# Kernel tuning notes

Hardware: AMD Instinct MI355X
Metric: run time of the kernel (lower is better)

Reference implementation:

```python
import jax, jax.numpy as jnp
import numpy as np

B, D, N, M = 64, 128, 400, 50
H, KD = 8, 16
NCONV, K, PAD = 4, 7, 3
MAXTS = 10000.0


def _pe(l):
    # PositionEncoding: freqs/phases interleave sin/cos as sin(pos*f + phase)
    i = np.arange(D)
    freqs = MAXTS ** np.where(i % 2 == 0, -i / D, -(i - 1) / D)
    phases = np.where(i % 2 == 0, 0.0, np.pi / 2)
    pos = np.arange(l)
    return jnp.asarray(np.sin(pos[None, :] * freqs[:, None] + phases[:, None]).astype(np.float32))  # [D, l]


def _ln(x, g, b, eps=1e-6):
    # LayerNorm1d over channel dim of [B, D, L]; torch .std() is unbiased (ddof=1), divides by (std+eps)
    mu = x.mean(axis=1, keepdims=True)
    sd = x.std(axis=1, keepdims=True, ddof=1)
    return g[None, :, None] * (x - mu) / (sd + eps) + b[None, :, None]


def _attn(xT, mask, Wq, bq, Wk, bk, Wv, bv, Wo, bo):
    # xT: [B, L, D]; per-head linears vectorized over the head axis
    q = jnp.einsum('bld,hdk->bhlk', xT, Wq) + bq[None, :, None, :]
    k = jnp.einsum('bld,hdk->bhlk', xT, Wk) + bk[None, :, None, :]
    v = jnp.einsum('bld,hdk->bhlk', xT, Wv) + bv[None, :, None, :]
    sc = jnp.einsum('bhik,bhjk->bhij', q, k) / np.sqrt(KD)
    sc = sc - 1e30 * (1.0 - mask[:, None, None, :])  # mask over key positions
    a = jax.nn.softmax(sc, axis=-1)
    o = jnp.einsum('bhij,bhjk->bhik', a, v)
    o = o.transpose(0, 2, 1, 3).reshape(xT.shape[0], xT.shape[1], H * KD)
    return o @ Wo + bo


def _fwd(context_emb, question_emb, c_mask, q_mask, ln_g, ln_b, dw_w, dw_b, pw_w, pw_b,
         Wq, bq, Wk, bk, Wv, bv, Wo, bo, Wfc, bfc, cq_wc, cq_wq, cq_wm, cq_b):
    def block(x, mask):
        out = x + _pe(x.shape[2])[None]
        for i in range(NCONV):  # fixed small layer loop
            res = out
            h = _ln(out, ln_g, ln_b)
            h = jax.lax.conv_general_dilated(h, dw_w[i], (1,), [(PAD, PAD)],
                                             feature_group_count=D,
                                             dimension_numbers=('NCH', 'OIH', 'NCH')) + dw_b[i][None, :, None]
            h = jnp.einsum('bdl,ed->bel', h, pw_w[i]) + pw_b[i][None, :, None]
            out = jax.nn.relu(h) + res  # eval-mode layer_dropout = inputs + residual
        res = out
        h = _ln(out, ln_g, ln_b)
        h = _attn(h.transpose(0, 2, 1), mask, Wq, bq, Wk, bk, Wv, bv, Wo, bo)
        out = h.transpose(0, 2, 1) + res
        res = out
        h = _ln(out, ln_g, ln_b)
        h = jnp.einsum('bdl,ed->bel', h, Wfc) + bfc[None, :, None]
        return h + res

    C = block(context_emb, c_mask)
    Q = block(question_emb, q_mask)
    C2 = C.transpose(0, 2, 1)  # [B, N, D]
    Q2 = Q.transpose(0, 2, 1)  # [B, M, D]
    # Biaffine similarity W0([Q; C; Q*C]) decomposed (same math, no [B,N*M,3D] materialization)
    S = (C2 @ cq_wc)[:, :, None] + (Q2 @ cq_wq)[:, None, :] \
        + jnp.einsum('bnd,bmd->bnm', C2 * cq_wm, Q2) + cq_b[0]
    S_r = jax.nn.softmax(S - 1e30 * (1.0 - q_mask[:, None, :]), axis=2)
    S_c = jax.nn.softmax(S - 1e30 * (1.0 - c_mask[:, :, None]), axis=1)
    A = S_r @ Q2                                    # context-to-query [B, N, D]
    Bt = jnp.einsum('bnm,bkm->bnk', S_r, S_c) @ C2  # query-to-context (DCN style) [B, N, D]
    return jnp.concatenate([C2, A, C2 * A, C2 * Bt], axis=-1)  # [B, N, 4D]


def setup_inputs() -> dict:
    key = jax.random.key(0)
    ks = jax.random.split(key, 16)
    s = 1.0 / np.sqrt(D)
    return dict(
        context_emb=jax.random.normal(ks[0], (B, D, N), jnp.float32),
        question_emb=jax.random.normal(ks[1], (B, D, M), jnp.float32),
        c_mask=jnp.ones((B, N), jnp.float32),
        q_mask=jnp.ones((B, M), jnp.float32),
        ln_g=jnp.ones((D,), jnp.float32),
        ln_b=jnp.zeros((D,), jnp.float32),
        dw_w=jax.random.normal(ks[2], (NCONV, D, 1, K), jnp.float32) / np.sqrt(K),
        dw_b=jnp.zeros((NCONV, D), jnp.float32),
        pw_w=jax.random.normal(ks[3], (NCONV, D, D), jnp.float32) * s,
        pw_b=jnp.zeros((NCONV, D), jnp.float32),
        Wq=jax.random.normal(ks[4], (H, D, KD), jnp.float32) * s,
        bq=jnp.zeros((H, KD), jnp.float32),
        Wk=jax.random.normal(ks[5], (H, D, KD), jnp.float32) * s,
        bk=jnp.zeros((H, KD), jnp.float32),
        Wv=jax.random.normal(ks[6], (H, D, KD), jnp.float32) * s,
        bv=jnp.zeros((H, KD), jnp.float32),
        Wo=jax.random.normal(ks[7], (H * KD, D), jnp.float32) * s,
        bo=jnp.zeros((D,), jnp.float32),
        Wfc=jax.random.normal(ks[8], (D, D), jnp.float32) * s,
        bfc=jnp.zeros((D,), jnp.float32),
        cq_wc=jax.random.normal(ks[9], (D,), jnp.float32) * s,
        cq_wq=jax.random.normal(ks[10], (D,), jnp.float32) * s,
        cq_wm=jax.random.normal(ks[11], (D,), jnp.float32) * s,
        cq_b=jnp.zeros((1,), jnp.float32),
    )


def reference(context_emb, question_emb, c_mask, q_mask, ln_g, ln_b, dw_w, dw_b, pw_w, pw_b,
              Wq, bq, Wk, bk, Wv, bv, Wo, bo, Wfc, bfc, cq_wc, cq_wq, cq_wm, cq_b):
    return _fwd(context_emb, question_emb, c_mask, q_mask, ln_g, ln_b, dw_w, dw_b, pw_w, pw_b,
                Wq, bq, Wk, bk, Wv, bv, Wo, bo, Wfc, bfc, cq_wc, cq_wq, cq_wm, cq_b)
```

## Files before the change

### kernel.cpp

```cpp
#include <hip/hip_runtime.h>
#include <math.h>

#define BB 64
#define DD 128
#define NN 400
#define MM 50
#define HH 8
#define KDIM 16
#define NC 4
#define KW 7
#define CH 200

#define SZ_C (BB * DD * NN)
#define SZ_Q (BB * DD * MM)
#define SSTAT (BB * NN + BB * MM)

__global__ void k_transposeW(const float* __restrict__ pw_w, const float* __restrict__ Wo,
                             const float* __restrict__ Wfc, const float* __restrict__ Wq,
                             const float* __restrict__ Wk, const float* __restrict__ Wv,
                             float* __restrict__ Wcan) {
  int idx = blockIdx.x * 256 + threadIdx.x;
  if (idx >= 9 * 16384) return;
  int m = idx >> 14;
  int r = idx & 16383;
  int d = r >> 7, e = r & 127;
  float v;
  if (m < 4) v = pw_w[m * 16384 + e * 128 + d];
  else if (m == 4) v = Wo[d * 128 + e];
  else if (m == 5) v = Wfc[e * 128 + d];
  else {
    const float* W = (m == 6) ? Wq : (m == 7) ? Wk : Wv;
    v = W[((e >> 4) * 128 + d) * 16 + (e & 15)];
  }
  Wcan[idx] = v;
}

__global__ void k_pestats(const float* __restrict__ xC, const float* __restrict__ xQ,
                          float* __restrict__ yC, float* __restrict__ yQ,
                          float* __restrict__ mu, float* __restrict__ inv) {
  int blk = blockIdx.x;
  const float* x; float* y; int L, l0, b, soff;
  if (blk < 448) { b = blk / 7; l0 = (blk % 7) * 64; x = xC; y = yC; L = NN; soff = 0; }
  else { b = blk - 448; l0 = 0; x = xQ; y = yQ; L = MM; soff = BB * NN; }
  int tid = threadIdx.x;
  int ll = tid & 63;
  int dq = tid >> 6;
  int l = l0 + ll;
  __shared__ float s_sum[4][64], s_sq[4][64];
  float sum = 0.f, sq = 0.f;
  if (l < L) {
    const float* px = x + (size_t)b * DD * L + l;
    float* py = y + (size_t)b * DD * L + l;
    for (int d = dq * 32; d < dq * 32 + 32; ++d) {
      int de = d & ~1;
      float freq = __expf((float)de * (-9.210340371976184f / 128.0f));
      float ph = (d & 1) ? 1.5707963267948966f : 0.0f;
      float v = px[(size_t)d * L] + sinf((float)l * freq + ph);
      py[(size_t)d * L] = v;
      sum += v; sq += v * v;
    }
  }
  s_sum[dq][ll] = sum; s_sq[dq][ll] = sq;
  __syncthreads();
  if (dq == 0 && l < L) {
    float ts = s_sum[0][ll] + s_sum[1][ll] + s_sum[2][ll] + s_sum[3][ll];
    float tq = s_sq[0][ll] + s_sq[1][ll] + s_sq[2][ll] + s_sq[3][ll];
    float m = ts * (1.0f / 128.0f);
    float var = (tq - 128.0f * m * m) * (1.0f / 127.0f);
    float sd = sqrtf(fmaxf(var, 0.f));
    mu[soff + b * L + l] = m;
    inv[soff + b * L + l] = 1.0f / (sd + 1e-6f);
  }
}

__global__ __launch_bounds__(256, 2) void k_convgemm(
    const float* __restrict__ xC, const float* __restrict__ xQ,
    float* __restrict__ outC, float* __restrict__ outQ,
    const float* __restrict__ Wc, const float* __restrict__ pwb,
    const float* __restrict__ dww, const float* __restrict__ dwb,
    const float* __restrict__ muI, const float* __restrict__ invI,
    float* __restrict__ muO, float* __restrict__ invO,
    const float* __restrict__ g, const float* __restrict__ beta) {
  int blk = blockIdx.x;
  int b = blk >> 3, tile = blk & 7;
  const float* x; float* out; int L, l0, soff;
  if (tile < 7) { x = xC; out = outC; L = NN; l0 = tile * 64; soff = 0; }
  else { x = xQ; out = outQ; L = MM; l0 = 0; soff = BB * NN; }
  __shared__ float Wl[32 * 128];
  __shared__ float Xl[32 * 64];
  __shared__ float Sm[70], Si[70];
  int tid = threadIdx.x;
  const float* xb = x + (size_t)b * DD * L;
  for (int t = tid; t < 70; t += 256) {
    int gl = l0 + t - 3;
    bool ok = (gl >= 0 && gl < L);
    Sm[t] = ok ? muI[soff + b * L + gl] : 0.f;
    Si[t] = ok ? invI[soff + b * L + gl] : 0.f;
  }
  float acc[8][4];
  #pragma unroll
  for (int i = 0; i < 8; ++i)
    #pragma unroll
    for (int j = 0; j < 4; ++j) acc[i][j] = 0.f;
  __syncthreads();
  for (int kc = 0; kc < 4; ++kc) {
    int d0 = kc * 32;
    #pragma unroll
    for (int i = 0; i < 4; ++i) {
      int idx = i * 256 + tid;
      ((float4*)Wl)[idx] = ((const float4*)Wc)[(size_t)d0 * 32 + idx];
    }
    #pragma unroll
    for (int r = 0; r < 2; ++r) {
      int k = r * 16 + (tid >> 4);
      int d = d0 + k;
      int c0 = (tid & 15) * 4;
      const float* xrow = xb + (size_t)d * L;
      float gd = g[d], bd = beta[d];
      float wv[7];
      #pragma unroll
      for (int u = 0; u < 7; ++u) wv[u] = dww[d * 7 + u];
      float dbv = dwb[d];
      float xw[10];
      int gbase = l0 + c0 - 3;
      if (gbase >= 1 && gbase + 11 <= L && (((unsigned)(d * L + gbase - 1)) & 3u) == 0u) {
        const float4* p = (const float4*)&xrow[gbase - 1];
        float4 A = p[0], Bv = p[1], Cv = p[2];
        float xr[12] = {A.x, A.y, A.z, A.w, Bv.x, Bv.y, Bv.z, Bv.w, Cv.x, Cv.y, Cv.z, Cv.w};
        #pragma unroll
        for (int s = 0; s < 10; ++s)
          xw[s] = gd * (xr[s + 1] - Sm[c0 + s]) * Si[c0 + s] + bd;
      } else {
        #pragma unroll
        for (int s = 0; s < 10; ++s) {
          int gl = gbase + s;
          float v = 0.f;
          if (gl >= 0 && gl < L)
            v = gd * (xrow[gl] - Sm[c0 + s]) * Si[c0 + s] + bd;
          xw[s] = v;
        }
      }
      float4 o;
      o.x = dbv; o.y = dbv; o.z = dbv; o.w = dbv;
      #pragma unroll
      for (int u = 0; u < 7; ++u) {
        o.x += wv[u] * xw[u];
        o.y += wv[u] * xw[u + 1];
        o.z += wv[u] * xw[u + 2];
        o.w += wv[u] * xw[u + 3];
      }
      *(float4*)&Xl[k * 64 + c0] = o;
    }
    __syncthreads();
    int e0 = (tid >> 4) * 8, cq = (tid & 15) * 4;
    for (int k = 0; k < 32; ++k) {
      const float4* wp = (const float4*)&Wl[k * 128 + e0];
      float4 w0 = wp[0], w1 = wp[1];
      float4 xv = *(const float4*)&Xl[k * 64 + cq];
      float we[8] = {w0.x, w0.y, w0.z, w0.w, w1.x, w1.y, w1.z, w1.w};
      float xe[4] = {xv.x, xv.y, xv.z, xv.w};
      #pragma unroll
      for (int i = 0; i < 8; ++i)
        #pragma unroll
        for (int j = 0; j < 4; ++j) acc[i][j] += we[i] * xe[j];
    }
    __syncthreads();
  }
  int e0 = (tid >> 4) * 8, cq = (tid & 15) * 4;
  float ssum[4], ssq[4];
  #pragma unroll
  for (int j = 0; j < 4; ++j) { ssum[j] = 0.f; ssq[j] = 0.f; }
  #pragma unroll
  for (int i = 0; i < 8; ++i) {
    float bi = pwb[e0 + i];
    float* po = out + ((size_t)b * DD + e0 + i) * L;
    const float* pr = xb + (size_t)(e0 + i) * L;
    #pragma unroll
    for (int j = 0; j < 4; ++j) {
      int l = l0 + cq + j;
      if (l < L) {
        float v = fmaxf(acc[i][j] + bi, 0.f) + pr[l];
        po[l] = v;
        ssum[j] += v; ssq[j] += v * v;
      }
    }
  }
  int grp = tid >> 4;
  #pragma unroll
  for (int j = 0; j < 4; ++j) {
    Xl[grp * 64 + cq + j] = ssum[j];
    Wl[grp * 64 + cq + j] = ssq[j];
  }
  __syncthreads();
  if (tid < 64) {
    int l = l0 + tid;
    if (l < L) {
      float ts = 0.f, tq = 0.f;
      #pragma unroll
      for (int gg = 0; gg < 16; ++gg) { ts += Xl[gg * 64 + tid]; tq += Wl[gg * 64 + tid]; }
      float m = ts * (1.0f / 128.0f);
      float var = (tq - 128.0f * m * m) * (1.0f / 127.0f);
      float sd = sqrtf(fmaxf(var, 0.f));
      muO[soff + b * L + l] = m;
      invO[soff + b * L + l] = 1.0f / (sd + 1e-6f);
    }
  }
}

template <int LNF, int ACT, int STATS>
__global__ __launch_bounds__(256) void k_gemm64(
    const float* __restrict__ xC, const float* __restrict__ xQ,
    float* __restrict__ outC, float* __restrict__ outQ,
    const float* __restrict__ Wc, const float* __restrict__ bias,
    const float* __restrict__ mu, const float* __restrict__ inv,
    float* __restrict__ muO, float* __restrict__ invO,
    const float* __restrict__ g, const float* __restrict__ beta) {
  int blk = blockIdx.x;
  int b = blk >> 3, tile = blk & 7;
  const float* x; float* out; int L, l0, soff;
  if (tile < 7) { x = xC; out = outC; L = NN; l0 = tile * 64; soff = 0; }
  else { x = xQ; out = outQ; L = MM; l0 = 0; soff = BB * NN; }
  __shared__ float Wl[32 * 128];
  __shared__ float Xl[32 * 64];
  int tid = threadIdx.x;
  float acc[8][4];
  #pragma unroll
  for (int i = 0; i < 8; ++i)
    #pragma unroll
    for (int j = 0; j < 4; ++j) acc[i][j] = 0.f;
  const float* xb = x + (size_t)b * DD * L;
  const float* pmu = mu + soff + b * L;
  const float* pin = inv + soff + b * L;
  for (int kc = 0; kc < 4; ++kc) {
    int d0 = kc * 32;
    #pragma unroll
    for (int i = 0; i < 4; ++i) {
      int idx = i * 256 + tid;
      ((float4*)Wl)[idx] = ((const float4*)Wc)[(size_t)d0 * 32 + idx];
    }
    #pragma unroll
    for (int t = 0; t < 8; ++t) {
      int idx = t * 256 + tid;
      int k = idx >> 6, l = idx & 63;
      float v = 0.f;
      int gl = l0 + l;
      if (gl < L) {
        v = xb[(size_t)(d0 + k) * L + gl];
        if (LNF) v = g[d0 + k] * (v - pmu[gl]) * pin[gl] + beta[d0 + k];
      }
      Xl[idx] = v;
    }
    __syncthreads();
    int e0 = (tid >> 4) * 8, cq = (tid & 15) * 4;
    for (int k = 0; k < 32; ++k) {
      const float4* wp = (const float4*)&Wl[k * 128 + e0];
      float4 w0 = wp[0], w1 = wp[1];
      float4 xv = *(const float4*)&Xl[k * 64 + cq];
      float we[8] = {w0.x, w0.y, w0.z, w0.w, w1.x, w1.y, w1.z, w1.w};
      float xe[4] = {xv.x, xv.y, xv.z, xv.w};
      #pragma unroll
      for (int i = 0; i < 8; ++i)
        #pragma unroll
        for (int j = 0; j < 4; ++j) acc[i][j] += we[i] * xe[j];
    }
    __syncthreads();
  }
  int e0 = (tid >> 4) * 8, cq = (tid & 15) * 4;
  float ssum[4], ssq[4];
  #pragma unroll
  for (int j = 0; j < 4; ++j) { ssum[j] = 0.f; ssq[j] = 0.f; }
  #pragma unroll
  for (int i = 0; i < 8; ++i) {
    float bi = bias[e0 + i];
    float* po = out + ((size_t)b * DD + e0 + i) * L;
    #pragma unroll
    for (int j = 0; j < 4; ++j) {
      int l = l0 + cq + j;
      if (l < L) {
        float v = acc[i][j] + bi;
        if (ACT != 0) v += po[l];
        po[l] = v;
        if (STATS) { ssum[j] += v; ssq[j] += v * v; }
      }
    }
  }
  if (STATS) {
    int grp = tid >> 4;
    #pragma unroll
    for (int j = 0; j < 4; ++j) {
      Xl[grp * 64 + cq + j] = ssum[j];
      Wl[grp * 64 + cq + j] = ssq[j];
    }
    __syncthreads();
    if (tid < 64) {
      int l = l0 + tid;
      if (l < L) {
        float ts = 0.f, tq = 0.f;
        #pragma unroll
        for (int gg = 0; gg < 16; ++gg) { ts += Xl[gg * 64 + tid]; tq += Wl[gg * 64 + tid]; }
        float m = ts * (1.0f / 128.0f);
        float var = (tq - 128.0f * m * m) * (1.0f / 127.0f);
        float sd = sqrtf(fmaxf(var, 0.f));
        muO[soff + b * L + l] = m;
        invO[soff + b * L + l] = 1.0f / (sd + 1e-6f);
      }
    }
  }
}

__global__ __launch_bounds__(256) void k_gemm_qkv(
    const float* __restrict__ xC, const float* __restrict__ xQ,
    float* __restrict__ o1C, float* __restrict__ o1Q,
    float* __restrict__ o2C, float* __restrict__ o2Q,
    float* __restrict__ o3C, float* __restrict__ o3Q,
    const float* __restrict__ Wcan,
    const float* __restrict__ bq, const float* __restrict__ bk, const float* __restrict__ bv,
    const float* __restrict__ mu, const float* __restrict__ inv,
    const float* __restrict__ g, const float* __restrict__ beta) {
  int blk0 = blockIdx.x;
  int grp = blk0 >> 9;
  int blk = blk0 & 511;
  const float* Wc = Wcan + (size_t)(6 + grp) * 16384;
  const float* bias = (grp == 0) ? bq : (grp == 1) ? bk : bv;
  float* oC = (grp == 0) ? o1C : (grp == 1) ? o2C : o3C;
  float* oQ = (grp == 0) ? o1Q : (grp == 1) ? o2Q : o3Q;
  int b = blk >> 3, tile = blk & 7;
  const float* x; float* out; int L, l0, soff;
  if (tile < 7) { x = xC; out = oC; L = NN; l0 = tile * 64; soff = 0; }
  else { x = xQ; out = oQ; L = MM; l0 = 0; soff = BB * NN; }
  __shared__ float Wl[32 * 128];
  __shared__ float Xl[32 * 64];
  int tid = threadIdx.x;
  float acc[8][4];
  #pragma unroll
  for (int i = 0; i < 8; ++i)
    #pragma unroll
    for (int j = 0; j < 4; ++j) acc[i][j] = 0.f;
  const float* xb = x + (size_t)b * DD * L;
  const float* pmu = mu + soff + b * L;
  const float* pin = inv + soff + b * L;
  for (int kc = 0; kc < 4; ++kc) {
    int d0 = kc * 32;
    #pragma unroll
    for (int i = 0; i < 4; ++i) {
      int idx = i * 256 + tid;
      ((float4*)Wl)[idx] = ((const float4*)Wc)[(size_t)d0 * 32 + idx];
    }
    #pragma unroll
    for (int t = 0; t < 8; ++t) {
      int idx = t * 256 + tid;
      int k = idx >> 6, l = idx & 63;
      float v = 0.f;
      int gl = l0 + l;
      if (gl < L) {
        v = xb[(size_t)(d0 + k) * L + gl];
        v = g[d0 + k] * (v - pmu[gl]) * pin[gl] + beta[d0 + k];
      }
      Xl[idx] = v;
    }
    __syncthreads();
    int e0 = (tid >> 4) * 8, cq = (tid & 15) * 4;
    for (int k = 0; k < 32; ++k) {
      const float4* wp = (const float4*)&Wl[k * 128 + e0];
      float4 w0 = wp[0], w1 = wp[1];
      float4 xv = *(const float4*)&Xl[k * 64 + cq];
      float we[8] = {w0.x, w0.y, w0.z, w0.w, w1.x, w1.y, w1.z, w1.w};
      float xe[4] = {xv.x, xv.y, xv.z, xv.w};
      #pragma unroll
      for (int i = 0; i < 8; ++i)
        #pragma unroll
        for (int j = 0; j < 4; ++j) acc[i][j] += we[i] * xe[j];
    }
    __syncthreads();
  }
  int e0 = (tid >> 4) * 8, cq = (tid & 15) * 4;
  #pragma unroll
  for (int i = 0; i < 8; ++i) {
    float bi = bias[e0 + i];
    float* po = out + ((size_t)b * DD + e0 + i) * L;
    #pragma unroll
    for (int j = 0; j < 4; ++j) {
      int l = l0 + cq + j;
      if (l < L) po[l] = acc[i][j] + bi;
    }
  }
}

__global__ __launch_bounds__(256) void k_attn2(
    const float* __restrict__ qC, const float* __restrict__ kC, const float* __restrict__ vC,
    const float* __restrict__ qQ, const float* __restrict__ kQ, const float* __restrict__ vQ,
    const float* __restrict__ cmask, const float* __restrict__ qmask,
    float* __restrict__ oC, float* __restrict__ oQ) {
  int blk = blockIdx.x;
  const float *qp, *kp, *vp, *mk; float* op; int L, b, h, q0, qcnt;
  if (blk < 1024) {
    b = blk >> 4; h = (blk >> 1) & 7; int half = blk & 1;
    qp = qC; kp = kC; vp = vC; mk = cmask; op = oC; L = NN;
    q0 = half * 256; qcnt = half ? (NN - 256) : 256;
  } else {
    int bb = blk - 1024; b = bb >> 3; h = bb & 7;
    qp = qQ; kp = kQ; vp = vQ; mk = qmask; op = oQ; L = MM;
    q0 = 0; qcnt = MM;
  }
  __shared__ float Kl[CH * KDIM];
  __shared__ float Vl[CH * KDIM];
  __shared__ float Ml[CH + 8];
  int tid = threadIdx.x;
  size_t base = ((size_t)b * DD + h * KDIM) * L;
  bool act = tid < qcnt;
  int i = q0 + tid;
  float q[KDIM];
  #pragma unroll
  for (int t = 0; t < KDIM; ++t)
    q[t] = act ? qp[base + (size_t)t * L + i] * 0.25f : 0.f;
  float m = -1e30f, ls = 0.f;
  float acc[KDIM];
  #pragma unroll
  for (int t = 0; t < KDIM; ++t) acc[t] = 0.f;

  for (int c0 = 0; c0 < L; c0 += CH) {
    int ch = L - c0; if (ch > CH) ch = CH;
    int chp = (ch + 7) & ~7;
    const float* kpc = kp + base + c0;
    const float* vpc = vp + base + c0;
    for (int idx = tid; idx < KDIM * ch; idx += 256) {
      int t = idx / ch, j = idx - t * ch;
      Kl[j * KDIM + t] = kpc[(size_t)t * L + j];
      Vl[j * KDIM + t] = vpc[(size_t)t * L + j];
    }
    for (int idx = tid; idx < (chp - ch) * KDIM; idx += 256) {
      int j = ch + (idx >> 4), t = idx & 15;
      Kl[j * KDIM + t] = 0.f; Vl[j * KDIM + t] = 0.f;
    }
    for (int j = tid; j < chp; j += 256)
      Ml[j] = (j < ch) ? -1e30f * (1.0f - mk[b * L + c0 + j]) : -1e30f;
    __syncthreads();
    if (act) {
      for (int j0 = 0; j0 < chp; j0 += 8) {
        const float4* mp = (const float4*)&Ml[j0];
        float4 ma0 = mp[0], ma1 = mp[1];
        float mav[8] = {ma0.x, ma0.y, ma0.z, ma0.w, ma1.x, ma1.y, ma1.z, ma1.w};
        float s[8];
        #pragma unroll
        for (int jj = 0; jj < 8; ++jj) {
          const float4* kf = (const float4*)&Kl[(j0 + jj) * KDIM];
          float4 k0 = kf[0], k1 = kf[1], k2 = kf[2], k3 = kf[3];
          float da = q[0] * k0.x + q[1] * k0.y + q[2] * k0.z + q[3] * k0.w
                   + q[4] * k1.x + q[5] * k1.y + q[6] * k1.z + q[7] * k1.w;
          float db = q[8] * k2.x + q[9] * k2.y + q[10] * k2.z + q[11] * k2.w
                   + q[12] * k3.x + q[13] * k3.y + q[14] * k3.z + q[15] * k3.w;
          s[jj] = da + db + mav[jj];
        }
        float cm = s[0];
        #pragma unroll
        for (int jj = 1; jj < 8; ++jj) cm = fmaxf(cm, s[jj]);
        if (cm > m) {
          float sc = __expf(m - cm);
          ls *= sc;
          #pragma unroll
          for (int t = 0; t < KDIM; ++t) acc[t] *= sc;
          m = cm;
        }
        #pragma unroll
        for (int jj = 0; jj < 8; ++jj) {
          float p = __expf(s[jj] - m);
          ls += p;
          const float4* vf = (const float4*)&Vl[(j0 + jj) * KDIM];
          float4 v0 = vf[0], v1 = vf[1], v2 = vf[2], v3 = vf[3];
          acc[0] += p * v0.x;  acc[1] += p * v0.y;  acc[2] += p * v0.z;  acc[3] += p * v0.w;
          acc[4] += p * v1.x;  acc[5] += p * v1.y;  acc[6] += p * v1.z;  acc[7] += p * v1.w;
          acc[8] += p * v2.x;  acc[9] += p * v2.y;  acc[10] += p * v2.z; acc[11] += p * v2.w;
          acc[12] += p * v3.x; acc[13] += p * v3.y; acc[14] += p * v3.z; acc[15] += p * v3.w;
        }
      }
    }
    __syncthreads();
  }
  if (act) {
    float invl = 1.0f / ls;
    #pragma unroll
    for (int t = 0; t < KDIM; ++t)
      op[base + (size_t)t * L + i] = acc[t] * invl;
  }
}

__global__ void k_prep(const float* __restrict__ Cb, const float* __restrict__ Qb,
                       float* __restrict__ C2, float* __restrict__ Q2,
                       const float* __restrict__ wc, const float* __restrict__ wq,
                       float* __restrict__ cd, float* __restrict__ qd) {
  int blk = blockIdx.x, tid = threadIdx.x;
  if (blk < 3840) {
    const float* X; float* Y; int L, rem;
    if (blk < 3328) { X = Cb; Y = C2; L = NN; rem = blk; }
    else { X = Qb; Y = Q2; L = MM; rem = blk - 3328; }
    int ntl = (L + 31) / 32;
    int b = rem / (4 * ntl);
    int r2 = rem % (4 * ntl);
    int d0 = (r2 / ntl) * 32;
    int l0 = (r2 % ntl) * 32;
    __shared__ float T[32][33];
    int c = tid & 31, r8 = tid >> 5;
    const float* xb = X + (size_t)b * DD * L;
    #pragma unroll
    for (int k = 0; k < 4; ++k) {
      int r = r8 + k * 8;
      int l = l0 + c;
      T[r][c] = (l < L) ? xb[(size_t)(d0 + r) * L + l] : 0.f;
    }
    __syncthreads();
    float* yb = Y + (size_t)b * L * DD;
    #pragma unroll
    for (int k = 0; k < 4; ++k) {
      int rr = r8 + k * 8;
      int l = l0 + rr;
      if (l < L) yb[(size_t)l * DD + d0 + c] = T[c][rr];
    }
  } else if (blk < 3940) {
    int idx = (blk - 3840) * 256 + tid;
    if (idx < BB * NN) {
      int l = idx % NN, b = idx / NN;
      const float* px = Cb + (size_t)b * DD * NN + l;
      float acc = 0.f;
      for (int d = 0; d < DD; ++d) acc += px[(size_t)d * NN] * wc[d];
      cd[idx] = acc;
    }
  } else {
    int idx = (blk - 3940) * 256 + tid;
    if (idx < BB * MM) {
      int l = idx % MM, b = idx / MM;
      const float* px = Qb + (size_t)b * DD * MM + l;
      float acc = 0.f;
      for (int d = 0; d < DD; ++d) acc += px[(size_t)d * MM] * wq[d];
      qd[idx] = acc;
    }
  }
}

__global__ void k_S(const float* __restrict__ C2, const float* __restrict__ Q2,
                    const float* __restrict__ cd, const float* __restrict__ qd,
                    const float* __restrict__ wm, const float* __restrict__ bias,
                    float* __restrict__ S) {
  int idx = blockIdx.x * 256 + threadIdx.x;
  if (idx >= BB * NN * MM) return;
  int mcol = idx % MM;
  int n = (idx / MM) % NN;
  int b = idx / (MM * NN);
  const float4* pc = (const float4*)(C2 + ((size_t)b * NN + n) * DD);
  const float4* pq = (const float4*)(Q2 + ((size_t)b * MM + mcol) * DD);
  const float4* pw = (const float4*)wm;
  float a0 = 0.f, a1 = 0.f;
  #pragma unroll 4
  for (int d4 = 0; d4 < 32; d4 += 2) {
    float4 c0 = pc[d4], w0 = pw[d4], q0 = pq[d4];
    float4 c1 = pc[d4 + 1], w1 = pw[d4 + 1], q1 = pq[d4 + 1];
    a0 += (c0.x * w0.x) * q0.x + (c0.y * w0.y) * q0.y + (c0.z * w0.z) * q0.z + (c0.w * w0.w) * q0.w;
    a1 += (c1.x * w1.x) * q1.x + (c1.y * w1.y) * q1.y + (c1.z * w1.z) * q1.z + (c1.w * w1.w) * q1.w;
  }
  S[idx] = a0 + a1 + cd[b * NN + n] + qd[b * MM + mcol] + bias[0];
}

__global__ void k_smax(const float* __restrict__ S, float* __restrict__ Sr,
                       float* __restrict__ Sc, const float* __restrict__ cmask,
                       const float* __restrict__ qmask) {
  int blk = blockIdx.x;
  int tid = threadIdx.x;
  if (blk < BB * MM) {
    int b = blk / MM;
    int mcol = blk % MM;
    float vals[7];
    float mx = -1e30f;
    #pragma unroll
    for (int c = 0; c < 7; ++c) {
      int n = tid + c * 64;
      float s = -1e30f;
      if (n < NN)
        s = S[((size_t)b * NN + n) * MM + mcol] - 1e30f * (1.0f - cmask[b * NN + n]);
      vals[c] = s;
      mx = fmaxf(mx, s);
    }
    #pragma unroll
    for (int off = 1; off < 64; off <<= 1) mx = fmaxf(mx, __shfl_xor(mx, off));
    float sum = 0.f;
    #pragma unroll
    for (int c = 0; c < 7; ++c) { vals[c] = __expf(vals[c] - mx); sum += vals[c]; }
    #pragma unroll
    for (int off = 1; off < 64; off <<= 1) sum += __shfl_xor(sum, off);
    float inv = 1.0f / sum;
    #pragma unroll
    for (int c = 0; c < 7; ++c) {
      int n = tid + c * 64;
      if (n < NN) Sc[((size_t)b * NN + n) * MM + mcol] = vals[c] * inv;
    }
  } else {
    int bn = blk - BB * MM;
    int b = bn / NN;
    float s = -1e30f;
    if (tid < MM)
      s = S[(size_t)bn * MM + tid] - 1e30f * (1.0f - qmask[b * MM + tid]);
    float mx = s;
    #pragma unroll
    for (int off = 1; off < 64; off <<= 1) mx = fmaxf(mx, __shfl_xor(mx, off));
    float e = (tid < MM) ? __expf(s - mx) : 0.f;
    float sum = e;
    #pragma unroll
    for (int off = 1; off < 64; off <<= 1) sum += __shfl_xor(sum, off);
    if (tid < MM) Sr[(size_t)bn * MM + tid] = e / sum;
  }
}

__global__ void k_U(const float* __restrict__ Sc, const float* __restrict__ C2,
                    float* __restrict__ U) {
  int idx = blockIdx.x * 256 + threadIdx.x;
  if (idx >= BB * MM * 32) return;
  int d4 = idx & 31;
  int rest = idx >> 5;
  int mcol = rest % MM;
  int b = rest / MM;
  const float* psc = Sc + (size_t)b * NN * MM + mcol;
  const float4* pc2 = (const float4*)(C2 + (size_t)b * NN * DD) + d4;
  float4 acc = {0.f, 0.f, 0.f, 0.f};
  #pragma unroll 4
  for (int kk = 0; kk < NN; ++kk) {
    float s = psc[(size_t)kk * MM];
    float4 c = pc2[(size_t)kk * 32];
    acc.x += s * c.x; acc.y += s * c.y; acc.z += s * c.z; acc.w += s * c.w;
  }
  ((float4*)U)[idx] = acc;
}

__global__ __launch_bounds__(256) void k_ABtF(
    const float* __restrict__ Sr, const float* __restrict__ Q2,
    const float* __restrict__ Uu, const float* __restrict__ C2,
    float* __restrict__ out) {
  int blk = blockIdx.x;
  int b = blk / 7, nt = blk % 7;
  int n0 = nt * 64;
  int nv = NN - n0; if (nv > 64) nv = 64;
  __shared__ float Ql[MM * 128];
  __shared__ float Ul[MM * 128];
  __shared__ float Sl[64 * MM];
  int tid = threadIdx.x;
  const float4* q4 = (const float4*)(Q2 + (size_t)b * MM * DD);
  const float4* u4 = (const float4*)(Uu + (size_t)b * MM * DD);
  for (int i = tid; i < MM * 32; i += 256) {
    ((float4*)Ql)[i] = q4[i];
    ((float4*)Ul)[i] = u4[i];
  }
  for (int i = tid; i < 64 * MM; i += 256) {
    int n = i / MM;
    Sl[i] = (n < nv) ? Sr[((size_t)b * NN + n0 + n) * MM + (i - n * MM)] : 0.f;
  }
  __syncthreads();
  int n = tid >> 2;
  if (n >= nv) return;
  int d04 = (tid & 3) * 8;
  float4 accA[8], accB[8];
  #pragma unroll
  for (int r = 0; r < 8; ++r) {
    accA[r] = {0.f, 0.f, 0.f, 0.f};
    accB[r] = {0.f, 0.f, 0.f, 0.f};
  }
  const float* sp = &Sl[n * MM];
  for (int m = 0; m < MM; ++m) {
    float s = sp[m];
    const float4* qp = (const float4*)&Ql[m * 128] + d04;
    const float4* up = (const float4*)&Ul[m * 128] + d04;
    #pragma unroll
    for (int r = 0; r < 8; ++r) {
      float4 q = qp[r], u = up[r];
      accA[r].x += s * q.x; accA[r].y += s * q.y; accA[r].z += s * q.z; accA[r].w += s * q.w;
      accB[r].x += s * u.x; accB[r].y += s * u.y; accB[r].z += s * u.z; accB[r].w += s * u.w;
    }
  }
  int gn = n0 + n;
  const float4* c4 = (const float4*)(C2 + ((size_t)b * NN + gn) * DD) + d04;
  float4* po = (float4*)(out + (size_t)(b * NN + gn) * 512);
  #pragma unroll
  for (int r = 0; r < 8; ++r) {
    float4 c = c4[r];
    float4 a = accA[r], bt = accB[r];
    po[d04 + r] = c;
    po[32 + d04 + r] = a;
    float4 ca = {c.x * a.x, c.y * a.y, c.z * a.z, c.w * a.w};
    po[64 + d04 + r] = ca;
    float4 cb = {c.x * bt.x, c.y * bt.y, c.z * bt.z, c.w * bt.w};
    po[96 + d04 + r] = cb;
  }
}

extern "C" void kernel_launch(void* const* d_in, const int* in_sizes, int n_in,
                              void* d_out, int out_size, void* d_ws, size_t ws_size,
                              hipStream_t stream) {
  (void)in_sizes; (void)n_in; (void)out_size; (void)ws_size;
  const float* ctx   = (const float*)d_in[0];
  const float* que   = (const float*)d_in[1];
  const float* cmask = (const float*)d_in[2];
  const float* qmask = (const float*)d_in[3];
  const float* ln_g  = (const float*)d_in[4];
  const float* ln_b  = (const float*)d_in[5];
  const float* dw_w  = (const float*)d_in[6];
  const float* dw_b  = (const float*)d_in[7];
  const float* pw_w  = (const float*)d_in[8];
  const float* pw_b  = (const float*)d_in[9];
  const float* Wq    = (const float*)d_in[10];
  const float* bq    = (const float*)d_in[11];
  const float* Wk    = (const float*)d_in[12];
  const float* bk    = (const float*)d_in[13];
  const float* Wv    = (const float*)d_in[14];
  const float* bv    = (const float*)d_in[15];
  const float* Wo    = (const float*)d_in[16];
  const float* bo    = (const float*)d_in[17];
  const float* Wfc   = (const float*)d_in[18];
  const float* bfc   = (const float*)d_in[19];
  const float* cq_wc = (const float*)d_in[20];
  const float* cq_wq = (const float*)d_in[21];
  const float* cq_wm = (const float*)d_in[22];
  const float* cq_b  = (const float*)d_in[23];
  float* out = (float*)d_out;
  float* ws = (float*)d_ws;

  float* Cb   = ws;
  float* Qb   = Cb + SZ_C;
  float* t1C  = Qb + SZ_Q;
  float* t1Q  = t1C + SZ_C;
  float* t2C  = t1Q + SZ_Q;
  float* t2Q  = t2C + SZ_C;
  float* t3C  = t2Q + SZ_Q;
  float* t3Q  = t3C + SZ_C;
  float* t4C  = t3Q + SZ_Q;
  float* t4Q  = t4C + SZ_C;
  float* mu0  = t4Q + SZ_Q;
  float* inv0 = mu0 + SSTAT;
  float* mu1  = inv0 + SSTAT;
  float* inv1 = mu1 + SSTAT;
  float* Wcan = inv1 + SSTAT;

  k_transposeW<<<(9 * 16384 + 255) / 256, 256, 0, stream>>>(pw_w, Wo, Wfc, Wq, Wk, Wv, Wcan);
  k_pestats<<<512, 256, 0, stream>>>(ctx, que, Cb, Qb, mu0, inv0);

  for (int i = 0; i < NC; ++i) {
    const float* inC = (i & 1) ? t1C : Cb;
    const float* inQ = (i & 1) ? t1Q : Qb;
    float* oC = (i & 1) ? Cb : t1C;
    float* oQ = (i & 1) ? Qb : t1Q;
    const float* mI = (i & 1) ? mu1 : mu0;
    const float* iI = (i & 1) ? inv1 : inv0;
    float* mO = (i & 1) ? mu0 : mu1;
    float* iO = (i & 1) ? inv0 : inv1;
    k_convgemm<<<512, 256, 0, stream>>>(inC, inQ, oC, oQ,
                                        Wcan + (size_t)i * 16384, pw_b + (size_t)i * DD,
                                        dw_w + (size_t)i * DD * KW, dw_b + (size_t)i * DD,
                                        mI, iI, mO, iO, ln_g, ln_b);
  }
  k_gemm_qkv<<<1536, 256, 0, stream>>>(Cb, Qb, t1C, t1Q, t2C, t2Q, t3C, t3Q,
                                       Wcan, bq, bk, bv, mu0, inv0, ln_g, ln_b);
  k_attn2<<<1536, 256, 0, stream>>>(t1C, t2C, t3C, t1Q, t2Q, t3Q, cmask, qmask, t4C, t4Q);
  k_gemm64<0, 1, 1><<<512, 256, 0, stream>>>(t4C, t4Q, Cb, Qb, Wcan + 4 * 16384, bo,
                                             mu0, inv0, mu1, inv1, ln_g, ln_b);
  k_gemm64<1, 1, 0><<<512, 256, 0, stream>>>(Cb, Qb, Cb, Qb, Wcan + 5 * 16384, bfc,
                                             mu1, inv1, mu0, inv0, ln_g, ln_b);

  float* C2  = t1C;
  float* Q2  = t1Q;
  float* S   = t2C;
  float* Sr  = t2C + 1638400;
  float* Scb = t3C;
  float* Uu  = t2Q;
  float* cd  = t3Q;
  float* qd  = t4Q;

  k_prep<<<3953, 256, 0, stream>>>(Cb, Qb, C2, Q2, cq_wc, cq_wq, cd, qd);
  k_S<<<(BB * NN * MM + 255) / 256, 256, 0, stream>>>(C2, Q2, cd, qd, cq_wm, cq_b, S);
  k_smax<<<BB * MM + BB * NN, 64, 0, stream>>>(S, Sr, Scb, cmask, qmask);
  k_U<<<(BB * MM * 32 + 255) / 256, 256, 0, stream>>>(Scb, C2, Uu);
  k_ABtF<<<448, 256, 0, stream>>>(Sr, Q2, Uu, C2, out);
}
```

Baseline: 718.2 us.

## Process two queries per thread in attention; tile trilinear similarity through shared memory

The attention kernel now gives each thread two query rows (i and i+256), so one block covers a full 400-length context head. Every K/V element loaded into shared memory is reused for two queries, and the grid shrinks from 1536 to 1024 blocks. The similarity kernel k_S is replaced by a tiled k_S2 that stages a 64-row context tile (pre-multiplied by wm) and all question rows in shared memory. Each thread then computes 13 outputs, instead of each thread re-reading full global rows for a single output. The trade-off is higher register pressure and lower occupancy in attention, and threads whose second query is out of range (i2 >= L) still do the second query's arithmetic as wasted work.

Result: slower. 734.4 us (+2.3%).

```diff
diff --git a/kernel.cpp b/kernel.cpp
--- a/kernel.cpp
+++ b/kernel.cpp
@@ -392,31 +392,31 @@
     const float* __restrict__ cmask, const float* __restrict__ qmask,
     float* __restrict__ oC, float* __restrict__ oQ) {
   int blk = blockIdx.x;
-  const float *qp, *kp, *vp, *mk; float* op; int L, b, h, q0, qcnt;
-  if (blk < 1024) {
-    b = blk >> 4; h = (blk >> 1) & 7; int half = blk & 1;
+  const float *qp, *kp, *vp, *mk; float* op; int L, b, h;
+  if (blk < 512) {
+    b = blk >> 3; h = blk & 7;
     qp = qC; kp = kC; vp = vC; mk = cmask; op = oC; L = NN;
-    q0 = half * 256; qcnt = half ? (NN - 256) : 256;
   } else {
-    int bb = blk - 1024; b = bb >> 3; h = bb & 7;
+    int bb = blk - 512; b = bb >> 3; h = bb & 7;
     qp = qQ; kp = kQ; vp = vQ; mk = qmask; op = oQ; L = MM;
-    q0 = 0; qcnt = MM;
   }
   __shared__ float Kl[CH * KDIM];
   __shared__ float Vl[CH * KDIM];
   __shared__ float Ml[CH + 8];
   int tid = threadIdx.x;
   size_t base = ((size_t)b * DD + h * KDIM) * L;
-  bool act = tid < qcnt;
-  int i = q0 + tid;
-  float q[KDIM];
-  #pragma unroll
-  for (int t = 0; t < KDIM; ++t)
-    q[t] = act ? qp[base + (size_t)t * L + i] * 0.25f : 0.f;
-  float m = -1e30f, ls = 0.f;
-  float acc[KDIM];
-  #pragma unroll
-  for (int t = 0; t < KDIM; ++t) acc[t] = 0.f;
+  int i1 = tid, i2 = tid + 256;
+  bool a1 = i1 < L, a2 = i2 < L;
+  float q1[KDIM], q2[KDIM];
+  #pragma unroll
+  for (int t = 0; t < KDIM; ++t) {
+    q1[t] = a1 ? qp[base + (size_t)t * L + i1] * 0.25f : 0.f;
+    q2[t] = a2 ? qp[base + (size_t)t * L + i2] * 0.25f : 0.f;
+  }
+  float m1 = -1e30f, m2 = -1e30f, ls1 = 0.f, ls2 = 0.f;
+  float acc1[KDIM], acc2[KDIM];
+  #pragma unroll
+  for (int t = 0; t < KDIM; ++t) { acc1[t] = 0.f; acc2[t] = 0.f; }
 
   for (int c0 = 0; c0 < L; c0 += CH) {
     int ch = L - c0; if (ch > CH) ch = CH;
@@ -435,52 +435,75 @@
     for (int j = tid; j < chp; j += 256)
       Ml[j] = (j < ch) ? -1e30f * (1.0f - mk[b * L + c0 + j]) : -1e30f;
     __syncthreads();
-    if (act) {
+    if (a1) {
       for (int j0 = 0; j0 < chp; j0 += 8) {
         const float4* mp = (const float4*)&Ml[j0];
         float4 ma0 = mp[0], ma1 = mp[1];
         float mav[8] = {ma0.x, ma0.y, ma0.z, ma0.w, ma1.x, ma1.y, ma1.z, ma1.w};
-        float s[8];
+        float s1[8], s2[8];
         #pragma unroll
         for (int jj = 0; jj < 8; ++jj) {
           const float4* kf = (const float4*)&Kl[(j0 + jj) * KDIM];
           float4 k0 = kf[0], k1 = kf[1], k2 = kf[2], k3 = kf[3];
-          float da = q[0] * k0.x + q[1] * k0.y + q[2] * k0.z + q[3] * k0.w
-                   + q[4] * k1.x + q[5] * k1.y + q[6] * k1.z + q[7] * k1.w;
-          float db = q[8] * k2.x + q[9] * k2.y + q[10] * k2.z + q[11] * k2.w
-                   + q[12] * k3.x + q[13] * k3.y + q[14] * k3.z + q[15] * k3.w;
-          s[jj] = da + db + mav[jj];
+          float d1a = q1[0] * k0.x + q1[1] * k0.y + q1[2] * k0.z + q1[3] * k0.w
+                    + q1[4] * k1.x + q1[5] * k1.y + q1[6] * k1.z + q1[7] * k1.w;
+          float d1b = q1[8] * k2.x + q1[9] * k2.y + q1[10] * k2.z + q1[11] * k2.w
+                    + q1[12] * k3.x + q1[13] * k3.y + q1[14] * k3.z + q1[15] * k3.w;
+          float d2a = q2[0] * k0.x + q2[1] * k0.y + q2[2] * k0.z + q2[3] * k0.w
+                    + q2[4] * k1.x + q2[5] * k1.y + q2[6] * k1.z + q2[7] * k1.w;
+          float d2b = q2[8] * k2.x + q2[9] * k2.y + q2[10] * k2.z + q2[11] * k2.w
+                    + q2[12] * k3.x + q2[13] * k3.y + q2[14] * k3.z + q2[15] * k3.w;
+          s1[jj] = d1a + d1b + mav[jj];
+          s2[jj] = d2a + d2b + mav[jj];
         }
-        float cm = s[0];
+        float cm1 = s1[0], cm2 = s2[0];
         #pragma unroll
-        for (int jj = 1; jj < 8; ++jj) cm = fmaxf(cm, s[jj]);
-        if (cm > m) {
-          float sc = __expf(m - cm);
-          ls *= sc;
+        for (int jj = 1; jj < 8; ++jj) { cm1 = fmaxf(cm1, s1[jj]); cm2 = fmaxf(cm2, s2[jj]); }
+        if (cm1 > m1) {
+          float sc = __expf(m1 - cm1);
+          ls1 *= sc;
           #pragma unroll
-          for (int t = 0; t < KDIM; ++t) acc[t] *= sc;
-          m = cm;
+          for (int t = 0; t < KDIM; ++t) acc1[t] *= sc;
+          m1 = cm1;
+        }
+        if (cm2 > m2) {
+          float sc = __expf(m2 - cm2);
+          ls2 *= sc;
+          #pragma unroll
+          for (int t = 0; t < KDIM; ++t) acc2[t] *= sc;
+          m2 = cm2;
         }
         #pragma unroll
         for (int jj = 0; jj < 8; ++jj) {
-          float p = __expf(s[jj] - m);
-          ls += p;
+          float p1 = __expf(s1[jj] - m1);
+          float p2 = __expf(s2[jj] - m2);
+          ls1 += p1; ls2 += p2;
           const float4* vf = (const float4*)&Vl[(j0 + jj) * KDIM];
           float4 v0 = vf[0], v1 = vf[1], v2 = vf[2], v3 = vf[3];
-          acc[0] += p * v0.x;  acc[1] += p * v0.y;  acc[2] += p * v0.z;  acc[3] += p * v0.w;
-          acc[4] += p * v1.x;  acc[5] += p * v1.y;  acc[6] += p * v1.z;  acc[7] += p * v1.w;
-          acc[8] += p * v2.x;  acc[9] += p * v2.y;  acc[10] += p * v2.z; acc[11] += p * v2.w;
-          acc[12] += p * v3.x; acc[13] += p * v3.y; acc[14] += p * v3.z; acc[15] += p * v3.w;
+          acc1[0] += p1 * v0.x;  acc1[1] += p1 * v0.y;  acc1[2] += p1 * v0.z;  acc1[3] += p1 * v0.w;
+          acc1[4] += p1 * v1.x;  acc1[5] += p1 * v1.y;  acc1[6] += p1 * v1.z;  acc1[7] += p1 * v1.w;
+          acc1[8] += p1 * v2.x;  acc1[9] += p1 * v2.y;  acc1[10] += p1 * v2.z; acc1[11] += p1 * v2.w;
+          acc1[12] += p1 * v3.x; acc1[13] += p1 * v3.y; acc1[14] += p1 * v3.z; acc1[15] += p1 * v3.w;
+          acc2[0] += p2 * v0.x;  acc2[1] += p2 * v0.y;  acc2[2] += p2 * v0.z;  acc2[3] += p2 * v0.w;
+          acc2[4] += p2 * v1.x;  acc2[5] += p2 * v1.y;  acc2[6] += p2 * v1.z;  acc2[7] += p2 * v1.w;
+          acc2[8] += p2 * v2.x;  acc2[9] += p2 * v2.y;  acc2[10] += p2 * v2.z; acc2[11] += p2 * v2.w;
+          acc2[12] += p2 * v3.x; acc2[13] += p2 * v3.y; acc2[14] += p2 * v3.z; acc2[15] += p2 * v3.w;
         }
       }
     }
     __syncthreads();
   }
-  if (act) {
-    float invl = 1.0f / ls;
+  if (a1) {
+    float invl = 1.0f / ls1;
     #pragma unroll
     for (int t = 0; t < KDIM; ++t)
-      op[base + (size_t)t * L + i] = acc[t] * invl;
+      op[base + (size_t)t * L + i1] = acc1[t] * invl;
+  }
+  if (a2) {
+    float invl = 1.0f / ls2;
+    #pragma unroll
+    for (int t = 0; t < KDIM; ++t)
+      op[base + (size_t)t * L + i2] = acc2[t] * invl;
   }
 }
 
@@ -536,27 +559,65 @@
   }
 }
 
-__global__ void k_S(const float* __restrict__ C2, const float* __restrict__ Q2,
-                    const float* __restrict__ cd, const float* __restrict__ qd,
-                    const float* __restrict__ wm, const float* __restrict__ bias,
-                    float* __restrict__ S) {
-  int idx = blockIdx.x * 256 + threadIdx.x;
-  if (idx >= BB * NN * MM) return;
-  int mcol = idx % MM;
-  int n = (idx / MM) % NN;
-  int b = idx / (MM * NN);
-  const float4* pc = (const float4*)(C2 + ((size_t)b * NN + n) * DD);
-  const float4* pq = (const float4*)(Q2 + ((size_t)b * MM + mcol) * DD);
-  const float4* pw = (const float4*)wm;
-  float a0 = 0.f, a1 = 0.f;
-  #pragma unroll 4
-  for (int d4 = 0; d4 < 32; d4 += 2) {
-    float4 c0 = pc[d4], w0 = pw[d4], q0 = pq[d4];
-    float4 c1 = pc[d4 + 1], w1 = pw[d4 + 1], q1 = pq[d4 + 1];
-    a0 += (c0.x * w0.x) * q0.x + (c0.y * w0.y) * q0.y + (c0.z * w0.z) * q0.z + (c0.w * w0.w) * q0.w;
-    a1 += (c1.x * w1.x) * q1.x + (c1.y * w1.y) * q1.y + (c1.z * w1.z) * q1.z + (c1.w * w1.w) * q1.w;
-  }
-  S[idx] = a0 + a1 + cd[b * NN + n] + qd[b * MM + mcol] + bias[0];
+__global__ __launch_bounds__(256) void k_S2(
+    const float* __restrict__ C2, const float* __restrict__ Q2,
+    const float* __restrict__ cd, const float* __restrict__ qd,
+    const float* __restrict__ wm, const float* __restrict__ bias,
+    float* __restrict__ S) {
+  int blk = blockIdx.x;
+  int b = blk / 7, nt = blk % 7;
+  int n0 = nt * 64;
+  int nv = NN - n0; if (nv > 64) nv = 64;
+  __shared__ float Cw[64 * 132];
+  __shared__ float Ql[52 * 132];
+  __shared__ float cdl[64];
+  __shared__ float qdl[50];
+  int tid = threadIdx.x;
+  const float4* c4g = (const float4*)(C2 + (size_t)b * NN * DD);
+  const float4* q4g = (const float4*)(Q2 + (size_t)b * MM * DD);
+  const float4* w4 = (const float4*)wm;
+  for (int i = tid; i < 64 * 32; i += 256) {
+    int n = i >> 5, d4 = i & 31;
+    float4 v = {0.f, 0.f, 0.f, 0.f};
+    if (n < nv) {
+      float4 c = c4g[(size_t)(n0 + n) * 32 + d4];
+      float4 w = w4[d4];
+      v.x = c.x * w.x; v.y = c.y * w.y; v.z = c.z * w.z; v.w = c.w * w.w;
+    }
+    *(float4*)&Cw[n * 132 + d4 * 4] = v;
+  }
+  for (int i = tid; i < 52 * 32; i += 256) {
+    int m = i >> 5, d4 = i & 31;
+    float4 v = {0.f, 0.f, 0.f, 0.f};
+    if (m < MM) v = q4g[(size_t)m * 32 + d4];
+    *(float4*)&Ql[m * 132 + d4 * 4] = v;
+  }
+  if (tid < 64) cdl[tid] = (tid < nv) ? cd[b * NN + n0 + tid] : 0.f;
+  if (tid >= 64 && tid < 114) qdl[tid - 64] = qd[b * MM + (tid - 64)];
+  __syncthreads();
+  int n = tid >> 2, mg = tid & 3;
+  int m0 = mg * 13;
+  float acc[13];
+  #pragma unroll
+  for (int k = 0; k < 13; ++k) acc[k] = 0.f;
+  const float* cp = &Cw[n * 132];
+  for (int d4 = 0; d4 < 32; ++d4) {
+    float4 c = *(const float4*)&cp[d4 * 4];
+    #pragma unroll
+    for (int k = 0; k < 13; ++k) {
+      float4 q = *(const float4*)&Ql[(m0 + k) * 132 + d4 * 4];
+      acc[k] += c.x * q.x + c.y * q.y + c.z * q.z + c.w * q.w;
+    }
+  }
+  if (n < nv) {
+    float add = cdl[n] + bias[0];
+    float* ps = S + ((size_t)b * NN + n0 + n) * MM + m0;
+    #pragma unroll
+    for (int k = 0; k < 13; ++k) {
+      int m = m0 + k;
+      if (m < MM) ps[k] = acc[k] + add + qdl[m];
+    }
+  }
 }
 
 __global__ void k_smax(const float* __restrict__ S, float* __restrict__ Sr,
@@ -754,7 +815,7 @@
   }
   k_gemm_qkv<<<1536, 256, 0, stream>>>(Cb, Qb, t1C, t1Q, t2C, t2Q, t3C, t3Q,
                                        Wcan, bq, bk, bv, mu0, inv0, ln_g, ln_b);
-  k_attn2<<<1536, 256, 0, stream>>>(t1C, t2C, t3C, t1Q, t2Q, t3Q, cmask, qmask, t4C, t4Q);
+  k_attn2<<<1024, 256, 0, stream>>>(t1C, t2C, t3C, t1Q, t2Q, t3Q, cmask, qmask, t4C, t4Q);
   k_gemm64<0, 1, 1><<<512, 256, 0, stream>>>(t4C, t4Q, Cb, Qb, Wcan + 4 * 16384, bo,
                                              mu0, inv0, mu1, inv1, ln_g, ln_b);
   k_gemm64<1, 1, 0><<<512, 256, 0, stream>>>(Cb, Qb, Cb, Qb, Wcan + 5 * 16384, bfc,
@@ -770,7 +831,7 @@
   float* qd  = t4Q;
 
   k_prep<<<3953, 256, 0, stream>>>(Cb, Qb, C2, Q2, cq_wc, cq_wq, cd, qd);
-  k_S<<<(BB * NN * MM + 255) / 256, 256, 0, stream>>>(C2, Q2, cd, qd, cq_wm, cq_b, S);
+  k_S2<<<448, 256, 0, stream>>>(C2, Q2, cd, qd, cq_wm, cq_b, S);
   k_smax<<<BB * MM + BB * NN, 64, 0, stream>>>(S, Sr, Scb, cmask, qmask);
   k_U<<<(BB * MM * 32 + 255) / 256, 256, 0, stream>>>(Scb, C2, Uu);
   k_ABtF<<<448, 256, 0, stream>>>(Sr, Q2, Uu, C2, out);
```
